# Performance work log

Hardware: AMD Instinct MI355X
Metric: run time of the kernel (lower is better)

Reference implementation:

```python
import jax, jax.numpy as jnp
import numpy as np

H = 1.0  # RBF bandwidth (init kwarg h)


def setup_inputs() -> dict:
    key = jax.random.key(0)
    k1, k2 = jax.random.split(key)
    x = jax.random.normal(k1, (8192, 512), dtype=jnp.float32)
    x1 = jax.random.normal(k2, (8192, 512), dtype=jnp.float32)
    return {"x": x, "x1": x1}


def reference(x, x1):
    # exp(-||x_i - x1_j||^2 / h), computed via the GEMM trick to avoid the
    # O(N*M*D) broadcast intermediate the original torch code materializes.
    x_sq = jnp.sum(x * x, axis=-1, keepdims=True)          # [N, 1]
    x1_sq = jnp.sum(x1 * x1, axis=-1)                       # [M]
    cross = jnp.einsum('nd,md->nm', x, x1)                  # [N, M]
    d = jnp.maximum(x_sq + x1_sq[None, :] - 2.0 * cross, 0.0)
    return jnp.exp(-d / H)
```

## Files before the change

kernel.cpp:

```cpp
#include <hip/hip_runtime.h>
#include <stdint.h>
#include <stddef.h>


#define NROWS 8192
#define DIMK  512
#define BM    128
#define BN    128
#define BKB   128
#define KT    (DIMK / BKB)

typedef __bf16 bf16x8 __attribute__((ext_vector_type(8)));
typedef int    i32x8  __attribute__((ext_vector_type(8)));
typedef int    i32x4  __attribute__((ext_vector_type(4)));
typedef float  f32x4  __attribute__((ext_vector_type(4)));

#define AS1 __attribute__((address_space(1)))
#define AS3 __attribute__((address_space(3)))

#define WAITV(n) asm volatile("s_waitcnt vmcnt(" #n ")" ::: "memory")
#define WAITL()  asm volatile("s_waitcnt lgkmcnt(0)" ::: "memory")
#define BAR()    asm volatile("s_barrier" ::: "memory")

__device__ __forceinline__ uint32_t f2bf(float f) {
    uint32_t u = __float_as_uint(f);
    return (u + 0x7FFFu + ((u >> 16) & 1u)) >> 16;
}

__device__ __forceinline__ uint32_t pk_fp8x4(float a, float b, float c, float d) {
    int w = __builtin_amdgcn_cvt_pk_fp8_f32(a, b, 0, false);
    w     = __builtin_amdgcn_cvt_pk_fp8_f32(c, d, w, true);
    return (uint32_t)w;
}

__device__ __forceinline__ i32x8 ld_frag(const uint8_t* base, int c_lo, int c_hi) {
    i32x4 lo = *(const i32x4*)(base + c_lo);
    i32x4 hi = *(const i32x4*)(base + c_hi);
    i32x8 r;
    r[0] = lo[0]; r[1] = lo[1]; r[2] = lo[2]; r[3] = lo[3];
    r[4] = hi[0]; r[5] = hi[1]; r[6] = hi[2]; r[7] = hi[3];
    return r;
}

__global__ __launch_bounds__(256) void precast_fp8(
    const float* __restrict__ x, const float* __restrict__ x1,
    uint8_t* __restrict__ xf, uint8_t* __restrict__ x1f,
    float* __restrict__ xsq, float* __restrict__ x1sq)
{
    const int w    = threadIdx.x >> 6;
    const int lane = threadIdx.x & 63;
    const int row  = blockIdx.x * 4 + w;
    const float* src;
    uint8_t* dstb;
    float* dsts;
    if (blockIdx.y == 0) { src = x  + (size_t)row * DIMK; dstb = xf  + (size_t)row * DIMK; dsts = xsq  + row; }
    else                 { src = x1 + (size_t)row * DIMK; dstb = x1f + (size_t)row * DIMK; dsts = x1sq + row; }

    float4 v0 = ((const float4*)src)[lane * 2];
    float4 v1 = ((const float4*)src)[lane * 2 + 1];
    float s = v0.x * v0.x + v0.y * v0.y + v0.z * v0.z + v0.w * v0.w
            + v1.x * v1.x + v1.y * v1.y + v1.z * v1.z + v1.w * v1.w;

    uint2 p;
    p.x = pk_fp8x4(v0.x, v0.y, v0.z, v0.w);
    p.y = pk_fp8x4(v1.x, v1.y, v1.z, v1.w);
    ((uint2*)dstb)[lane] = p;

    #pragma unroll
    for (int off = 32; off > 0; off >>= 1) s += __shfl_down(s, off);
    if (lane == 0) *dsts = s;
}

__global__ __launch_bounds__(256) void norms_only(
    const float* __restrict__ x, const float* __restrict__ x1,
    float* __restrict__ xsq, float* __restrict__ x1sq)
{
    const int row = blockIdx.x;
    const float* src = (blockIdx.y == 0) ? x + (size_t)row * DIMK : x1 + (size_t)row * DIMK;
    float* dsts      = (blockIdx.y == 0) ? xsq + row : x1sq + row;
    const int t = threadIdx.x;
    float2 v = ((const float2*)src)[t];
    float s = v.x * v.x + v.y * v.y;
    #pragma unroll
    for (int off = 32; off > 0; off >>= 1) s += __shfl_down(s, off);
    __shared__ float red[4];
    if ((t & 63) == 0) red[t >> 6] = s;
    __syncthreads();
    if (t == 0) *dsts = red[0] + red[1] + red[2] + red[3];
}

__global__ __launch_bounds__(512, 4) void rbf_mfma_mxfp8(
    const uint8_t* __restrict__ Xf, const uint8_t* __restrict__ X1f,
    const float* __restrict__ xsq, const float* __restrict__ x1sq,
    float* __restrict__ out)
{
    __shared__ uint8_t lds[65536];

    const int t    = threadIdx.x;
    const int id   = blockIdx.x;
    const int xcd  = id & 7;
    const int loc  = id >> 3;
    const int bm   = loc >> 3;
    const int bn   = (xcd << 3) | (loc & 7);
    const int lane = t & 63;
    const int w    = t >> 6;
    const int wm   = w >> 2;
    const int wn   = w & 3;

    const int srow   = t >> 3;
    const int schunk = (t & 7) ^ (srow & 7);
    const uint8_t* gA = Xf  + (size_t)(bm * BM + srow) * DIMK + schunk * 16;
    const uint8_t* gB = X1f + (size_t)(bn * BN + srow) * DIMK + schunk * 16;

    f32x4 acc[2][4];
    #pragma unroll
    for (int i = 0; i < 2; ++i)
        #pragma unroll
        for (int j = 0; j < 4; ++j)
            acc[i][j] = f32x4{0.f, 0.f, 0.f, 0.f};

    const int lrow = lane & 15;
    const int q    = lane >> 4;
    const int s    = lrow & 7;
    const int c_lo = ((2 * q)     ^ s) * 16;
    const int c_hi = ((2 * q + 1) ^ s) * 16;

    auto stage = [&](int kt, int b) {
        const uint8_t* ga = gA + kt * BKB;
        const uint8_t* gb = gB + kt * BKB;
        uint8_t* la = &lds[b * 16384 + t * 16];
        uint8_t* lb = &lds[32768 + b * 16384 + t * 16];
        #pragma unroll
        for (int c = 0; c < 2; ++c) {
            __builtin_amdgcn_global_load_lds((AS1 void*)(ga + (size_t)c * 64 * DIMK),
                                             (AS3 void*)(la + c * 8192), 16, 0, 0);
            __builtin_amdgcn_global_load_lds((AS1 void*)(gb + (size_t)c * 64 * DIMK),
                                             (AS3 void*)(lb + c * 8192), 16, 0, 0);
        }
    };

    auto read_frags = [&](int b, i32x8* af, i32x8* bg) {
        const uint8_t* Ab = &lds[b * 16384 + wm * 64 * BKB];
        const uint8_t* Bb = &lds[32768 + b * 16384 + wn * 32 * BKB];
        #pragma unroll
        for (int i = 0; i < 4; ++i) af[i] = ld_frag(Ab + (i * 16 + lrow) * BKB, c_lo, c_hi);
        #pragma unroll
        for (int i = 0; i < 2; ++i) bg[i] = ld_frag(Bb + (i * 16 + lrow) * BKB, c_lo, c_hi);
    };

    auto do_mfma = [&](const i32x8* af, const i32x8* bg) {
        #pragma unroll
        for (int j = 0; j < 2; ++j)
            #pragma unroll
            for (int i = 0; i < 4; ++i)
                acc[j][i] = __builtin_amdgcn_mfma_scale_f32_16x16x128_f8f6f4(
                    bg[j], af[i], acc[j][i],
                    0, 0,
                    0, 0x7F7F7F7F,
                    0, 0x7F7F7F7F);
    };

    i32x8 af[4], bg[2];

    stage(0, 0);
    stage(1, 1);

    WAITV(4); BAR();
    read_frags(0, af, bg);
    WAITL(); BAR();
    stage(2, 0);
    do_mfma(af, bg);

    WAITV(4); BAR();
    read_frags(1, af, bg);
    WAITL(); BAR();
    stage(3, 1);
    do_mfma(af, bg);

    WAITV(4); BAR();
    read_frags(0, af, bg);
    do_mfma(af, bg);

    WAITV(0); BAR();
    read_frags(1, af, bg);
    do_mfma(af, bg);

    const int orow_w = bm * BM + wm * 64;
    const int ocol_w = bn * BN + wn * 32;
    uint8_t* scr = &lds[w * 2048];

    float xsl[4];
    f32x4 x1v[2];
    #pragma unroll
    for (int tm = 0; tm < 4; ++tm) xsl[tm] = xsq[orow_w + tm * 16 + lrow];
    #pragma unroll
    for (int tn = 0; tn < 2; ++tn) x1v[tn] = *(const f32x4*)&x1sq[ocol_w + tn * 16 + q * 4];

    const int crow = lane >> 3;
    const int clc  = lane & 7;

    #pragma unroll
    for (int tm = 0; tm < 4; ++tm) {
        #pragma unroll
        for (int tn = 0; tn < 2; ++tn) {
            f32x4 a = acc[tn][tm];
            f32x4 ev;
            #pragma unroll
            for (int r = 0; r < 4; ++r) {
                float d = fmaxf(xsl[tm] + x1v[tn][r] - 2.0f * a[r], 0.0f);
                ev[r] = __expf(-d);
            }
            const int lc = tn * 4 + q;
            *(f32x4*)(scr + lrow * 128 + ((lc ^ s) * 16)) = ev;
        }
        float* gbase = out + (size_t)(orow_w + tm * 16) * NROWS + ocol_w;
        #pragma unroll
        for (int si = 0; si < 2; ++si) {
            const int row = si * 8 + crow;
            f32x4 v = *(const f32x4*)(scr + row * 128 + ((clc ^ (row & 7)) * 16));
            __builtin_nontemporal_store(v, (f32x4*)(gbase + (size_t)row * NROWS + clc * 4));
        }
    }
}

#define FBM 128
#define FBN 128
__global__ __launch_bounds__(256) void rbf_mfma_inline(
    const float* __restrict__ X, const float* __restrict__ X1,
    const float* __restrict__ xsq, const float* __restrict__ x1sq,
    float* __restrict__ out)
{
    __shared__ uint16_t As[FBM * 32];
    __shared__ uint16_t Bs[FBN * 32];

    const int t    = threadIdx.x;
    const int bm   = blockIdx.x;
    const int bn   = blockIdx.y;
    const int lane = t & 63;
    const int w    = t >> 6;
    const int wm   = w >> 1;
    const int wn   = w & 1;

    f32x4 acc[4][4];
    #pragma unroll
    for (int i = 0; i < 4; ++i)
        #pragma unroll
        for (int j = 0; j < 4; ++j)
            acc[i][j] = f32x4{0.f, 0.f, 0.f, 0.f};

    const int lrow = lane & 15;
    const int kq   = (lane >> 4) * 8;
    int aoff[4], boff[4];
    #pragma unroll
    for (int i = 0; i < 4; ++i) {
        aoff[i] = (wm * 64 + i * 16 + lrow) * 32 + kq;
        boff[i] = (wn * 64 + i * 16 + lrow) * 32 + kq;
    }

    #pragma unroll 1
    for (int kt = 0; kt < DIMK / 32; ++kt) {
        #pragma unroll
        for (int i = 0; i < 4; ++i) {
            const int g   = t + i * 256;
            const int row = g >> 3;
            const int c4  = (g & 7) * 4;
            float4 va = *(const float4*)&X [(size_t)(bm * FBM + row) * DIMK + kt * 32 + c4];
            float4 vb = *(const float4*)&X1[(size_t)(bn * FBN + row) * DIMK + kt * 32 + c4];
            uint2 pa, pb;
            pa.x = f2bf(va.x) | (f2bf(va.y) << 16);
            pa.y = f2bf(va.z) | (f2bf(va.w) << 16);
            pb.x = f2bf(vb.x) | (f2bf(vb.y) << 16);
            pb.y = f2bf(vb.z) | (f2bf(vb.w) << 16);
            *(uint2*)&As[g * 4] = pa;
            *(uint2*)&Bs[g * 4] = pb;
        }
        __syncthreads();

        bf16x8 af[4], bg[4];
        #pragma unroll
        for (int i = 0; i < 4; ++i) af[i] = *(const bf16x8*)&As[aoff[i]];
        #pragma unroll
        for (int i = 0; i < 4; ++i) bg[i] = *(const bf16x8*)&Bs[boff[i]];
        #pragma unroll
        for (int i = 0; i < 4; ++i)
            #pragma unroll
            for (int j = 0; j < 4; ++j)
                acc[i][j] = __builtin_amdgcn_mfma_f32_16x16x32_bf16(af[i], bg[j], acc[i][j], 0, 0, 0);
        __syncthreads();
    }

    const int row0 = bm * FBM + wm * 64 + (lane >> 4) * 4;
    const int col0 = bn * FBN + wn * 64 + lrow;
    float xs[4][4], x1s[4];
    #pragma unroll
    for (int tm = 0; tm < 4; ++tm)
        #pragma unroll
        for (int r = 0; r < 4; ++r) xs[tm][r] = xsq[row0 + tm * 16 + r];
    #pragma unroll
    for (int tn = 0; tn < 4; ++tn) x1s[tn] = x1sq[col0 + tn * 16];

    #pragma unroll
    for (int tm = 0; tm < 4; ++tm)
        #pragma unroll
        for (int tn = 0; tn < 4; ++tn)
            #pragma unroll
            for (int r = 0; r < 4; ++r) {
                const int row = row0 + tm * 16 + r;
                const int col = col0 + tn * 16;
                float d = xs[tm][r] + x1s[tn] - 2.0f * acc[tm][tn][r];
                d = fmaxf(d, 0.0f);
                out[(size_t)row * NROWS + col] = __expf(-d);
            }
}

extern "C" void kernel_launch(void* const* d_in, const int* in_sizes, int n_in,
                              void* d_out, int out_size, void* d_ws, size_t ws_size,
                              hipStream_t stream)
{
    const float* x  = (const float*)d_in[0];
    const float* x1 = (const float*)d_in[1];
    float* out = (float*)d_out;

    const size_t f8_bytes  = (size_t)NROWS * DIMK;
    const size_t need_full = 2 * f8_bytes + 2 * (size_t)NROWS * sizeof(float);

    if (ws_size >= need_full) {
        uint8_t* xf   = (uint8_t*)d_ws;
        uint8_t* x1f  = xf + f8_bytes;
        float*   xsq  = (float*)((char*)d_ws + 2 * f8_bytes);
        float*   x1sq = xsq + NROWS;
        precast_fp8<<<dim3(NROWS / 4, 2), 256, 0, stream>>>(x, x1, xf, x1f, xsq, x1sq);
        rbf_mfma_mxfp8<<<(NROWS / BM) * (NROWS / BN), 512, 0, stream>>>(xf, x1f, xsq, x1sq, out);
    } else {
        float* xsq  = (float*)d_ws;
        float* x1sq = xsq + NROWS;
        norms_only<<<dim3(NROWS, 2), 256, 0, stream>>>(x, x1, xsq, x1sq);
        rbf_mfma_inline<<<dim3(NROWS / FBM, NROWS / FBN), 256, 0, stream>>>(x, x1, xsq, x1sq, out);
    }
}
```

Before: 296.5 us.

## Replace tiled fp8 GEMM with persistent kernel keeping A rows resident in LDS

```diff
diff --git a/kernel.cpp b/kernel.cpp
--- a/kernel.cpp
+++ b/kernel.cpp
@@ -5,10 +5,6 @@
 
 #define NROWS 8192
 #define DIMK  512
-#define BM    128
-#define BN    128
-#define BKB   128
-#define KT    (DIMK / BKB)
 
 typedef __bf16 bf16x8 __attribute__((ext_vector_type(8)));
 typedef int    i32x8  __attribute__((ext_vector_type(8)));
@@ -89,35 +85,23 @@
     if (t == 0) *dsts = red[0] + red[1] + red[2] + red[3];
 }
 
-__global__ __launch_bounds__(512, 4) void rbf_mfma_mxfp8(
+__global__ __launch_bounds__(256) void rbf_pers_mxfp8(
     const uint8_t* __restrict__ Xf, const uint8_t* __restrict__ X1f,
     const float* __restrict__ xsq, const float* __restrict__ x1sq,
     float* __restrict__ out)
 {
-    __shared__ uint8_t lds[65536];
+    __shared__ uint8_t lds[81920];
 
     const int t    = threadIdx.x;
     const int id   = blockIdx.x;
     const int xcd  = id & 7;
     const int loc  = id >> 3;
-    const int bm   = loc >> 3;
-    const int bn   = (xcd << 3) | (loc & 7);
+    const int rp   = (xcd << 4) | (loc & 15);
+    const int cq   = loc >> 4;
     const int lane = t & 63;
     const int w    = t >> 6;
-    const int wm   = w >> 2;
-    const int wn   = w & 3;
-
-    const int srow   = t >> 3;
-    const int schunk = (t & 7) ^ (srow & 7);
-    const uint8_t* gA = Xf  + (size_t)(bm * BM + srow) * DIMK + schunk * 16;
-    const uint8_t* gB = X1f + (size_t)(bn * BN + srow) * DIMK + schunk * 16;
-
-    f32x4 acc[2][4];
-    #pragma unroll
-    for (int i = 0; i < 2; ++i)
-        #pragma unroll
-        for (int j = 0; j < 4; ++j)
-            acc[i][j] = f32x4{0.f, 0.f, 0.f, 0.f};
+    const int wm   = w >> 1;
+    const int wn   = w & 1;
 
     const int lrow = lane & 15;
     const int q    = lane >> 4;
@@ -125,100 +109,117 @@
     const int c_lo = ((2 * q)     ^ s) * 16;
     const int c_hi = ((2 * q + 1) ^ s) * 16;
 
-    auto stage = [&](int kt, int b) {
-        const uint8_t* ga = gA + kt * BKB;
-        const uint8_t* gb = gB + kt * BKB;
-        uint8_t* la = &lds[b * 16384 + t * 16];
-        uint8_t* lb = &lds[32768 + b * 16384 + t * 16];
-        #pragma unroll
-        for (int c = 0; c < 2; ++c) {
-            __builtin_amdgcn_global_load_lds((AS1 void*)(ga + (size_t)c * 64 * DIMK),
-                                             (AS3 void*)(la + c * 8192), 16, 0, 0);
-            __builtin_amdgcn_global_load_lds((AS1 void*)(gb + (size_t)c * 64 * DIMK),
-                                             (AS3 void*)(lb + c * 8192), 16, 0, 0);
-        }
-    };
-
-    auto read_frags = [&](int b, i32x8* af, i32x8* bg) {
-        const uint8_t* Ab = &lds[b * 16384 + wm * 64 * BKB];
-        const uint8_t* Bb = &lds[32768 + b * 16384 + wn * 32 * BKB];
-        #pragma unroll
-        for (int i = 0; i < 4; ++i) af[i] = ld_frag(Ab + (i * 16 + lrow) * BKB, c_lo, c_hi);
-        #pragma unroll
-        for (int i = 0; i < 2; ++i) bg[i] = ld_frag(Bb + (i * 16 + lrow) * BKB, c_lo, c_hi);
-    };
-
-    auto do_mfma = [&](const i32x8* af, const i32x8* bg) {
-        #pragma unroll
-        for (int j = 0; j < 2; ++j)
-            #pragma unroll
-            for (int i = 0; i < 4; ++i)
-                acc[j][i] = __builtin_amdgcn_mfma_scale_f32_16x16x128_f8f6f4(
-                    bg[j], af[i], acc[j][i],
-                    0, 0,
-                    0, 0x7F7F7F7F,
-                    0, 0x7F7F7F7F);
-    };
-
-    i32x8 af[4], bg[2];
-
-    stage(0, 0);
-    stage(1, 1);
-
-    WAITV(4); BAR();
-    read_frags(0, af, bg);
-    WAITL(); BAR();
-    stage(2, 0);
-    do_mfma(af, bg);
-
-    WAITV(4); BAR();
-    read_frags(1, af, bg);
-    WAITL(); BAR();
-    stage(3, 1);
-    do_mfma(af, bg);
-
-    WAITV(4); BAR();
-    read_frags(0, af, bg);
-    do_mfma(af, bg);
-
-    WAITV(0); BAR();
-    read_frags(1, af, bg);
-    do_mfma(af, bg);
-
-    const int orow_w = bm * BM + wm * 64;
-    const int ocol_w = bn * BN + wn * 32;
-    uint8_t* scr = &lds[w * 2048];
-
-    float xsl[4];
-    f32x4 x1v[2];
-    #pragma unroll
-    for (int tm = 0; tm < 4; ++tm) xsl[tm] = xsq[orow_w + tm * 16 + lrow];
-    #pragma unroll
-    for (int tn = 0; tn < 2; ++tn) x1v[tn] = *(const f32x4*)&x1sq[ocol_w + tn * 16 + q * 4];
-
+    {
+        const uint8_t* gA = Xf + (size_t)rp * 64 * DIMK;
+        #pragma unroll
+        for (int c = 0; c < 8; ++c) {
+            const int g   = c * 256 + t;
+            const int r   = g >> 5;
+            const int off = r * DIMK + ((g & 24) << 4) + (((g & 7) ^ (r & 7)) << 4);
+            __builtin_amdgcn_global_load_lds((AS1 void*)(gA + off),
+                                             (AS3 void*)(&lds[(size_t)g * 16]), 16, 0, 0);
+        }
+    }
+
+    i32x4 breg[8];
+    {
+        const uint8_t* gB = X1f + (size_t)(cq * 32 + 0) * 64 * DIMK;
+        #pragma unroll
+        for (int c = 0; c < 8; ++c)
+            breg[c] = *(const i32x4*)(gB + (size_t)(c * 256 + t) * 16);
+    }
+
+    float xsl[2];
+    #pragma unroll
+    for (int fi = 0; fi < 2; ++fi)
+        xsl[fi] = xsq[rp * 64 + wm * 32 + fi * 16 + lrow];
+
+    f32x4 x1n[2];
+    #pragma unroll
+    for (int fj = 0; fj < 2; ++fj)
+        x1n[fj] = *(const f32x4*)&x1sq[(cq * 32 + 0) * 64 + wn * 32 + fj * 16 + q * 4];
+
+    uint8_t* scr = &lds[65536 + w * 4096];
     const int crow = lane >> 3;
     const int clc  = lane & 7;
 
-    #pragma unroll
-    for (int tm = 0; tm < 4; ++tm) {
-        #pragma unroll
-        for (int tn = 0; tn < 2; ++tn) {
-            f32x4 a = acc[tn][tm];
-            f32x4 ev;
-            #pragma unroll
-            for (int r = 0; r < 4; ++r) {
-                float d = fmaxf(xsl[tm] + x1v[tn][r] - 2.0f * a[r], 0.0f);
-                ev[r] = __expf(-d);
+    #pragma unroll 1
+    for (int i = 0; i < 32; ++i) {
+        BAR();
+        WAITV(2);
+
+        f32x4 x1v0 = x1n[0], x1v1 = x1n[1];
+
+        #pragma unroll
+        for (int c = 0; c < 8; ++c) {
+            const int g   = c * 256 + t;
+            const int r   = g >> 5;
+            const int dst = 32768 + r * DIMK + ((g & 24) << 4) + (((g & 7) ^ (r & 7)) << 4);
+            *(i32x4*)(&lds[dst]) = breg[c];
+        }
+        WAITL(); BAR();
+
+        {
+            const int ip = (i < 31) ? i + 1 : 31;
+            const uint8_t* gB = X1f + (size_t)(cq * 32 + ip) * 64 * DIMK;
+            #pragma unroll
+            for (int c = 0; c < 8; ++c)
+                breg[c] = *(const i32x4*)(gB + (size_t)(c * 256 + t) * 16);
+            #pragma unroll
+            for (int fj = 0; fj < 2; ++fj)
+                x1n[fj] = *(const f32x4*)&x1sq[(cq * 32 + ip) * 64 + wn * 32 + fj * 16 + q * 4];
+        }
+
+        f32x4 acc[2][2];
+        #pragma unroll
+        for (int a = 0; a < 2; ++a)
+            #pragma unroll
+            for (int b = 0; b < 2; ++b)
+                acc[a][b] = f32x4{0.f, 0.f, 0.f, 0.f};
+
+        #pragma unroll
+        for (int kt = 0; kt < 4; ++kt) {
+            i32x8 af[2], bg[2];
+            #pragma unroll
+            for (int fi = 0; fi < 2; ++fi)
+                af[fi] = ld_frag(&lds[(wm * 32 + fi * 16 + lrow) * DIMK + kt * 128], c_lo, c_hi);
+            #pragma unroll
+            for (int fj = 0; fj < 2; ++fj)
+                bg[fj] = ld_frag(&lds[32768 + (wn * 32 + fj * 16 + lrow) * DIMK + kt * 128], c_lo, c_hi);
+            #pragma unroll
+            for (int fj = 0; fj < 2; ++fj)
+                #pragma unroll
+                for (int fi = 0; fi < 2; ++fi)
+                    acc[fj][fi] = __builtin_amdgcn_mfma_scale_f32_16x16x128_f8f6f4(
+                        bg[fj], af[fi], acc[fj][fi],
+                        0, 0, 0, 0x7F7F7F7F, 0, 0x7F7F7F7F);
+        }
+
+        #pragma unroll
+        for (int fi = 0; fi < 2; ++fi)
+            #pragma unroll
+            for (int fj = 0; fj < 2; ++fj) {
+                f32x4 a  = acc[fj][fi];
+                f32x4 x1v = (fj == 0) ? x1v0 : x1v1;
+                f32x4 ev;
+                #pragma unroll
+                for (int r = 0; r < 4; ++r) {
+                    float d = fmaxf(xsl[fi] + x1v[r] - 2.0f * a[r], 0.0f);
+                    ev[r] = __expf(-d);
+                }
+                const int rl = fi * 16 + lrow;
+                const int lc = fj * 4 + q;
+                *(f32x4*)(scr + rl * 128 + ((lc ^ (rl & 7)) * 16)) = ev;
             }
-            const int lc = tn * 4 + q;
-            *(f32x4*)(scr + lrow * 128 + ((lc ^ s) * 16)) = ev;
-        }
-        float* gbase = out + (size_t)(orow_w + tm * 16) * NROWS + ocol_w;
-        #pragma unroll
-        for (int si = 0; si < 2; ++si) {
-            const int row = si * 8 + crow;
-            f32x4 v = *(const f32x4*)(scr + row * 128 + ((clc ^ (row & 7)) * 16));
-            __builtin_nontemporal_store(v, (f32x4*)(gbase + (size_t)row * NROWS + clc * 4));
+        {
+            float* gbase = out + (size_t)(rp * 64 + wm * 32) * NROWS
+                               + (size_t)(cq * 32 + i) * 64 + wn * 32;
+            #pragma unroll
+            for (int si = 0; si < 4; ++si) {
+                const int row = si * 8 + crow;
+                f32x4 v = *(const f32x4*)(scr + row * 128 + ((clc ^ (row & 7)) * 16));
+                __builtin_nontemporal_store(v, (f32x4*)(gbase + (size_t)row * NROWS + clc * 4));
+            }
         }
     }
 }
@@ -330,7 +331,7 @@
         float*   xsq  = (float*)((char*)d_ws + 2 * f8_bytes);
         float*   x1sq = xsq + NROWS;
         precast_fp8<<<dim3(NROWS / 4, 2), 256, 0, stream>>>(x, x1, xf, x1f, xsq, x1sq);
-        rbf_mfma_mxfp8<<<(NROWS / BM) * (NROWS / BN), 512, 0, stream>>>(xf, x1f, xsq, x1sq, out);
+        rbf_pers_mxfp8<<<512, 256, 0, stream>>>(xf, x1f, xsq, x1sq, out);
     } else {
         float* xsq  = (float*)d_ws;
         float* x1sq = xsq + NROWS;
```

Measured after the change: 326.4 us. 10.1% more time.
